# Kernel optimization log

Hardware: AMD Instinct MI355X
Metric: run time of the kernel (lower is better)

## Reference

```python
import jax, jax.numpy as jnp
import numpy as np

B, C, H, W = 8, 256, 64, 64
GROUPS = 8
EPS = 1e-5


def setup_inputs() -> dict:
    key = jax.random.key(0)
    ks = jax.random.split(key, 10)
    s = 1.0 / np.sqrt(C)
    return {
        "x": jax.random.normal(ks[0], (B, C, H, W), dtype=jnp.float32),
        "gn_gamma": jnp.ones((C,), jnp.float32),
        "gn_beta": jnp.zeros((C,), jnp.float32),
        "wq": jax.random.uniform(ks[1], (C, C), jnp.float32, -s, s),
        "bq": jax.random.uniform(ks[2], (C,), jnp.float32, -s, s),
        "wk": jax.random.uniform(ks[3], (C, C), jnp.float32, -s, s),
        "bk": jax.random.uniform(ks[4], (C,), jnp.float32, -s, s),
        "wv": jax.random.uniform(ks[5], (C, C), jnp.float32, -s, s),
        "bv": jax.random.uniform(ks[6], (C,), jnp.float32, -s, s),
        "wp": jax.random.uniform(ks[7], (C, C), jnp.float32, -s, s),
        "bp": jax.random.uniform(ks[8], (C,), jnp.float32, -s, s),
    }


def _group_norm(x, gamma, beta):
    b, c, h, w = x.shape
    xg = x.reshape(b, GROUPS, c // GROUPS, h, w)
    mu = jnp.mean(xg, axis=(2, 3, 4), keepdims=True)
    var = jnp.mean(jnp.square(xg - mu), axis=(2, 3, 4), keepdims=True)
    xn = ((xg - mu) * jax.lax.rsqrt(var + EPS)).reshape(b, c, h, w)
    return xn * gamma[None, :, None, None] + beta[None, :, None, None]


def reference(x, gn_gamma, gn_beta, wq, bq, wk, bk, wv, bv, wp, bp):
    b, c, h, w = x.shape
    xn = _group_norm(x, gn_gamma, gn_beta)
    xf = xn.reshape(b, c, h * w)  # [b, c, n]
    # 1x1 Conv1d == per-position channel matmul
    q = jnp.einsum('oc,bcn->bon', wq, xf) + bq[None, :, None]
    k = jnp.einsum('oc,bcn->bon', wk, xf) + bk[None, :, None]
    v = jnp.einsum('oc,bcn->bon', wv, xf) + bv[None, :, None]
    scale = 1.0 / jnp.sqrt(jnp.asarray(c, xf.dtype))
    # attn[b,i,j] = softmax_j(q[:,i]^T k[:,j] / sqrt(c))
    attn = jax.nn.softmax(jnp.einsum('bci,bcj->bij', q, k) * scale, axis=-1)
    # out[b,c,i] = sum_j v[b,c,j] * attn[b,i,j]
    out = jnp.einsum('bcj,bij->bci', v, attn)
    out = jnp.einsum('oc,bcn->bon', wp, out) + bp[None, :, None]
    return x + out.reshape(b, c, h, w)
```

## Files before the change

### kernel.cpp

```cpp
#include <hip/hip_runtime.h>


typedef __bf16 bf16x8 __attribute__((ext_vector_type(8)));
typedef __bf16 bf16x4 __attribute__((ext_vector_type(4)));
typedef float floatx4 __attribute__((ext_vector_type(4)));
typedef float floatx16 __attribute__((ext_vector_type(16)));

constexpr int Bb = 8, Cc_ = 256, HW = 4096;
constexpr int BNT = Bb * HW;

__device__ __forceinline__ void load_lds16(const void* g, void* l) {
  __builtin_amdgcn_global_load_lds((const __attribute__((address_space(1))) void*)g,
                                   (__attribute__((address_space(3))) void*)l, 16, 0, 0);
}

#define MEMFENCE asm volatile("" ::: "memory")
__device__ __forceinline__ void bar_sync() {
  MEMFENCE;
  __builtin_amdgcn_s_barrier();
  MEMFENCE;
}

__global__ __launch_bounds__(256) void gn_part(const float* __restrict__ x,
                                               float* __restrict__ part) {
  int sub = blockIdx.x & 7;
  int bg = blockIdx.x >> 3;
  const float4* p = (const float4*)(x + (size_t)bg * 131072 + (size_t)sub * 16384);
  int tid = threadIdx.x;
  float s = 0.f, ss = 0.f;
#pragma unroll
  for (int i = 0; i < 16; ++i) {
    float4 v = p[i * 256 + tid];
    s += v.x + v.y + v.z + v.w;
    ss += v.x * v.x + v.y * v.y + v.z * v.z + v.w * v.w;
  }
  for (int off = 32; off; off >>= 1) { s += __shfl_down(s, off); ss += __shfl_down(ss, off); }
  __shared__ float red[8];
  int wv = tid >> 6, ln = tid & 63;
  if (ln == 0) { red[wv] = s; red[4 + wv] = ss; }
  __syncthreads();
  if (tid == 0) {
    part[blockIdx.x * 2] = red[0] + red[1] + red[2] + red[3];
    part[blockIdx.x * 2 + 1] = red[4] + red[5] + red[6] + red[7];
  }
}

__global__ __launch_bounds__(256) void gn_norm_t(const float* __restrict__ x,
                                                 const float* __restrict__ part,
                                                 const float* __restrict__ gamma,
                                                 const float* __restrict__ beta,
                                                 __bf16* __restrict__ Xt) {
  __shared__ float tile[64][65];
  __shared__ float sst[4];
  int b = blockIdx.z, c0 = blockIdx.y * 64, n0 = blockIdx.x * 64;
  int tid = threadIdx.x;
  if (tid < 2) {
    int g = b * 8 + (c0 >> 5) + tid;
    float s = 0.f, ss = 0.f;
#pragma unroll
    for (int k = 0; k < 8; ++k) { s += part[(g * 8 + k) * 2]; ss += part[(g * 8 + k) * 2 + 1]; }
    float mean = s / 131072.f;
    float var = ss / 131072.f - mean * mean;
    sst[tid * 2] = mean;
    sst[tid * 2 + 1] = rsqrtf(var + 1e-5f);
  }
  int cl = tid >> 4, nl = (tid & 15) * 4;
  const float* xb = x + ((size_t)b * Cc_ + c0) * HW + n0;
#pragma unroll
  for (int i = 0; i < 4; ++i) {
    int c = cl + i * 16;
    float4 v = *(const float4*)&xb[(size_t)c * HW + nl];
    tile[c][nl] = v.x; tile[c][nl + 1] = v.y; tile[c][nl + 2] = v.z; tile[c][nl + 3] = v.w;
  }
  __syncthreads();
#pragma unroll
  for (int i = 0; i < 16; ++i) {
    int idx = i * 256 + tid;
    int n = idx >> 6, c = idx & 63;
    int gc = c0 + c;
    float mean = sst[(c >> 5) * 2], rstd = sst[(c >> 5) * 2 + 1];
    float v = (tile[c][n] - mean) * rstd * gamma[gc] + beta[gc];
    Xt[((size_t)b * HW + n0 + n) * Cc_ + gc] = (__bf16)v;
  }
}

__global__ __launch_bounds__(256) void pack_w(const float* __restrict__ wq, const float* __restrict__ wk,
                                              const float* __restrict__ wv, const float* __restrict__ wp,
                                              const float* __restrict__ bq, const float* __restrict__ bk,
                                              const float* __restrict__ bv, const float* __restrict__ bp,
                                              __bf16* __restrict__ Wqk, __bf16* __restrict__ Wv,
                                              __bf16* __restrict__ Wp, float* __restrict__ Bqk,
                                              float* __restrict__ Bv, float* __restrict__ Bp) {
  int i = blockIdx.x * 256 + threadIdx.x;
  if (i < 65536) {
    Wqk[i] = (__bf16)wq[i];
    Wqk[65536 + i] = (__bf16)wk[i];
    Wv[i] = (__bf16)wv[i];
    Wp[i] = (__bf16)wp[i];
  }
  if (i < 256) { Bqk[i] = bq[i]; Bqk[256 + i] = bk[i]; Bv[i] = bv[i]; Bp[i] = bp[i]; }
}

template <int BM, int BN, int WM, int WN, int EPI>
__global__ __launch_bounds__(256) void gemm_bt(
    const __bf16* __restrict__ A, int lda,
    const __bf16* __restrict__ B, int ldb,
    __bf16* __restrict__ C, int ldc,
    int K, float scale,
    const float* __restrict__ bias,
    const float* __restrict__ resid,
    float* __restrict__ outF) {
  constexpr int TM = WM / 16, TN = WN / 16;
  __shared__ __bf16 As[BM * 32];
  __shared__ __bf16 Bs[BN * 32];

  const int tid = threadIdx.x;
  const int wave = tid >> 6, lane = tid & 63;
  const int wr = wave >> 1, wc = wave & 1;
  const int quad = lane >> 4, l16 = lane & 15;
  const int m0 = blockIdx.y * BM, n0 = blockIdx.x * BN;
  const int srow = lane >> 2;
  const int scol = (lane & 3) * 8;

  floatx4 acc[TM][TN] = {};

  const int kTiles = K / 32;
  for (int kt = 0; kt < kTiles; ++kt) {
    const int k0 = kt * 32;
    __syncthreads();
#pragma unroll
    for (int i = 0; i < BM / 64; ++i) {
      int row = i * 64 + wave * 16 + srow;
      load_lds16(A + (size_t)(m0 + row) * lda + k0 + scol, &As[(i * 64 + wave * 16) * 32]);
    }
#pragma unroll
    for (int i = 0; i < BN / 64; ++i) {
      int row = i * 64 + wave * 16 + srow;
      load_lds16(B + (size_t)(n0 + row) * ldb + k0 + scol, &Bs[(i * 64 + wave * 16) * 32]);
    }
    __syncthreads();

    bf16x8 af[TM], bfr[TN];
#pragma unroll
    for (int i = 0; i < TM; ++i)
      af[i] = *(const bf16x8*)&As[(wr * WM + i * 16 + l16) * 32 + quad * 8];
#pragma unroll
    for (int j = 0; j < TN; ++j)
      bfr[j] = *(const bf16x8*)&Bs[(wc * WN + j * 16 + l16) * 32 + quad * 8];
#pragma unroll
    for (int i = 0; i < TM; ++i)
#pragma unroll
      for (int j = 0; j < TN; ++j)
        acc[i][j] = __builtin_amdgcn_mfma_f32_16x16x32_bf16(af[i], bfr[j], acc[i][j], 0, 0, 0);
  }

#pragma unroll
  for (int i = 0; i < TM; ++i) {
#pragma unroll
    for (int j = 0; j < TN; ++j) {
      int gc = n0 + wc * WN + j * 16 + l16;
#pragma unroll
      for (int r = 0; r < 4; ++r) {
        int gr = m0 + wr * WM + i * 16 + quad * 4 + r;
        float v = acc[i][j][r] * scale;
        if constexpr (EPI == 1) v += bias[gc];
        if constexpr (EPI == 2) v += bias[gr];
        if constexpr (EPI == 3) {
          int bb = gc >> 12, nn = gc & 4095;
          size_t oidx = (size_t)bb * (Cc_ * HW) + (size_t)gr * HW + nn;
          outF[oidx] = v + bias[gr] + resid[oidx];
        } else {
          C[(size_t)gr * ldc + gc] = (__bf16)v;
        }
      }
    }
  }
}

__global__ __launch_bounds__(256, 2) void flash_attn(const __bf16* __restrict__ QK,
                                                     const __bf16* __restrict__ V,
                                                     __bf16* __restrict__ O) {
  __shared__ __align__(16) __bf16 smem[40960];
  __bf16* Ks = smem;
  __bf16* Vt = smem + 16384;
  __bf16* Pb = smem + 32768;

  const int tid = threadIdx.x;
  const int w = tid >> 6, lane = tid & 63;
  const int l31 = lane & 31, hh = lane >> 5;
  const int b = blockIdx.x & 7;
  const int m0 = (blockIdx.x >> 3) * 64;

  if (w < 2) {
    const int h = w;
    const int ks_slot = lane & 31, ks_rin = lane >> 5;

    bf16x8 qf[2][16];
#pragma unroll
    for (int qt = 0; qt < 2; ++qt) {
      const size_t qrow = (size_t)(b * HW + m0 + qt * 32 + l31);
#pragma unroll
      for (int kc = 0; kc < 16; ++kc) {
        qf[qt][kc] = *(const bf16x8*)&QK[qrow * 512 + kc * 16 + hh * 8];
#pragma unroll
        for (int e = 0; e < 8; ++e) qf[qt][kc][e] = (__bf16)((float)qf[qt][kc][e] * 0.0625f);
      }
    }
#pragma unroll
    for (int i = 0; i < 16; ++i) {
      int rl = h * 32 + i * 2 + ks_rin;
      load_lds16(QK + (size_t)(b * HW + rl) * 512 + 256 + ((ks_slot ^ (rl & 31)) << 3),
                 &Ks[(h * 32 + i * 2) * 256]);
    }
    bar_sync();

    float lr0 = 0.f, lr1 = 0.f;
    const int jl = h * 32 + l31;
    const __bf16* krow = &Ks[jl * 256];
    const int jx = l31;

    for (int t = 0; t < 64; ++t) {
      asm volatile("s_waitcnt vmcnt(0)" ::: "memory");
      floatx16 s0 = {}, s1 = {};
      __builtin_amdgcn_s_setprio(1);
#pragma unroll
      for (int kc = 0; kc < 16; ++kc) {
        bf16x8 kfv = *(const bf16x8*)&krow[((kc * 2 + hh) ^ jx) << 3];
        s0 = __builtin_amdgcn_mfma_f32_32x32x16_bf16(kfv, qf[0][kc], s0, 0, 0, 0);
        s1 = __builtin_amdgcn_mfma_f32_32x32x16_bf16(kfv, qf[1][kc], s1, 0, 0, 0);
      }
      __builtin_amdgcn_s_setprio(0);
      asm volatile("s_waitcnt lgkmcnt(0)" ::: "memory");
      if (t < 63) {
#pragma unroll
        for (int i = 0; i < 16; ++i) {
          int rl = h * 32 + i * 2 + ks_rin;
          load_lds16(QK + (size_t)(b * HW + (t + 1) * 64 + rl) * 512 + 256 +
                         ((ks_slot ^ (rl & 31)) << 3),
                     &Ks[(h * 32 + i * 2) * 256]);
        }
      }
      float ls0 = 0.f, ls1 = 0.f;
#pragma unroll
      for (int i = 0; i < 16; ++i) {
        float p0 = __expf(s0[i]); s0[i] = p0; ls0 += p0;
        float p1 = __expf(s1[i]); s1[i] = p1; ls1 += p1;
      }
      lr0 += ls0; lr1 += ls1;
      __bf16* Pt = Pb + ((t & 1) << 12);
#pragma unroll
      for (int g = 0; g < 4; ++g) {
        bf16x4 pk0, pk1;
#pragma unroll
        for (int k = 0; k < 4; ++k) { pk0[k] = (__bf16)s0[g * 4 + k]; pk1[k] = (__bf16)s1[g * 4 + k]; }
        *(bf16x4*)&Pt[(l31) * 64 + ((((4 * h + g) ^ (l31 & 7)) << 3) + 4 * hh)] = pk0;
        *(bf16x4*)&Pt[(32 + l31) * 64 + ((((4 * h + g) ^ (l31 & 7)) << 3) + 4 * hh)] = pk1;
      }
      asm volatile("s_waitcnt lgkmcnt(0)" ::: "memory");
      bar_sync();
    }

    float* Lb = (float*)(smem + 32768);
    float l20 = lr0 + __shfl_xor(lr0, 32);
    float l21 = lr1 + __shfl_xor(lr1, 32);
    if (hh == 0) { Lb[h * 64 + l31] = l20; Lb[h * 64 + 32 + l31] = l21; }
    asm volatile("s_waitcnt lgkmcnt(0)" ::: "memory");
    bar_sync();
    if (w == 0) Lb[128 + lane] = 1.f / (Lb[lane] + Lb[64 + lane]);
    asm volatile("s_waitcnt lgkmcnt(0)" ::: "memory");
    bar_sync();
    bar_sync();
  } else {
    const int ch = w - 2;
    const int vt_slot = lane & 7, vt_rin = lane >> 3;

#pragma unroll
    for (int i = 0; i < 16; ++i) {
      int cl = ch * 128 + i * 8 + vt_rin;
      load_lds16(V + (size_t)cl * BNT + (b * HW + ((vt_slot ^ (cl & 7)) << 3)),
                 &Vt[(ch * 128 + i * 8) * 64]);
    }
    bar_sync();

    floatx16 oacc[2][4] = {};

    for (int t = 0; t < 64; ++t) {
      asm volatile("s_waitcnt vmcnt(0)" ::: "memory");
      if (t > 0) {
        const __bf16* Pp = Pb + (((t - 1) & 1) << 12);
        __builtin_amdgcn_s_setprio(1);
#pragma unroll
        for (int ks = 0; ks < 4; ++ks) {
          bf16x8 pf0 = *(const bf16x8*)&Pp[(l31) * 64 + (((ks * 2 + hh) ^ (l31 & 7)) << 3)];
          bf16x8 pf1 = *(const bf16x8*)&Pp[(32 + l31) * 64 + (((ks * 2 + hh) ^ (l31 & 7)) << 3)];
#pragma unroll
          for (int nt = 0; nt < 4; ++nt) {
            int cl = ch * 128 + nt * 32 + l31;
            bf16x8 vf = *(const bf16x8*)&Vt[cl * 64 + (((ks * 2 + hh) ^ (cl & 7)) << 3)];
            oacc[0][nt] = __builtin_amdgcn_mfma_f32_32x32x16_bf16(pf0, vf, oacc[0][nt], 0, 0, 0);
            oacc[1][nt] = __builtin_amdgcn_mfma_f32_32x32x16_bf16(pf1, vf, oacc[1][nt], 0, 0, 0);
          }
        }
        __builtin_amdgcn_s_setprio(0);
        asm volatile("s_waitcnt lgkmcnt(0)" ::: "memory");
#pragma unroll
        for (int i = 0; i < 16; ++i) {
          int cl = ch * 128 + i * 8 + vt_rin;
          load_lds16(V + (size_t)cl * BNT + (b * HW + t * 64 + ((vt_slot ^ (cl & 7)) << 3)),
                     &Vt[(ch * 128 + i * 8) * 64]);
        }
      }
      bar_sync();
    }

    asm volatile("s_waitcnt vmcnt(0)" ::: "memory");
    {
      const __bf16* Pp = Pb + 4096;
      __builtin_amdgcn_s_setprio(1);
#pragma unroll
      for (int ks = 0; ks < 4; ++ks) {
        bf16x8 pf0 = *(const bf16x8*)&Pp[(l31) * 64 + (((ks * 2 + hh) ^ (l31 & 7)) << 3)];
        bf16x8 pf1 = *(const bf16x8*)&Pp[(32 + l31) * 64 + (((ks * 2 + hh) ^ (l31 & 7)) << 3)];
#pragma unroll
        for (int nt = 0; nt < 4; ++nt) {
          int cl = ch * 128 + nt * 32 + l31;
          bf16x8 vf = *(const bf16x8*)&Vt[cl * 64 + (((ks * 2 + hh) ^ (cl & 7)) << 3)];
          oacc[0][nt] = __builtin_amdgcn_mfma_f32_32x32x16_bf16(pf0, vf, oacc[0][nt], 0, 0, 0);
          oacc[1][nt] = __builtin_amdgcn_mfma_f32_32x32x16_bf16(pf1, vf, oacc[1][nt], 0, 0, 0);
        }
      }
      __builtin_amdgcn_s_setprio(0);
    }
    asm volatile("s_waitcnt lgkmcnt(0)" ::: "memory");
    bar_sync();
    bar_sync();

    const float* Linv = (const float*)(smem + 32768) + 128;
    __bf16* Os = smem;
#pragma unroll
    for (int qt = 0; qt < 2; ++qt) {
#pragma unroll
      for (int g = 0; g < 4; ++g) {
        floatx4 lv = *(const floatx4*)&Linv[qt * 32 + g * 8 + 4 * hh];
#pragma unroll
        for (int k = 0; k < 4; ++k) {
          int qloc = qt * 32 + g * 8 + 4 * hh + k;
#pragma unroll
          for (int nt = 0; nt < 4; ++nt) {
            int c = ch * 128 + nt * 32 + l31;
            Os[qloc * 256 + c] = (__bf16)(oacc[qt][nt][g * 4 + k] * lv[k]);
          }
        }
      }
    }
    asm volatile("s_waitcnt lgkmcnt(0)" ::: "memory");
    bar_sync();
  }

  const float4* src = (const float4*)smem;
  float4* dst = (float4*)(O + (size_t)(b * HW + m0) * 256);
#pragma unroll
  for (int i = 0; i < 8; ++i) dst[i * 256 + tid] = src[i * 256 + tid];
}

extern "C" void kernel_launch(void* const* d_in, const int* in_sizes, int n_in,
                              void* d_out, int out_size, void* d_ws, size_t ws_size,
                              hipStream_t stream) {
  const float* x = (const float*)d_in[0];
  const float* gamma = (const float*)d_in[1];
  const float* beta = (const float*)d_in[2];
  const float* wq = (const float*)d_in[3];
  const float* bq = (const float*)d_in[4];
  const float* wk = (const float*)d_in[5];
  const float* bk = (const float*)d_in[6];
  const float* wv = (const float*)d_in[7];
  const float* bv = (const float*)d_in[8];
  const float* wp = (const float*)d_in[9];
  const float* bp = (const float*)d_in[10];
  float* out = (float*)d_out;

  char* ws = (char*)d_ws;
  size_t off = 0;
  auto alloc = [&](size_t n) { size_t o = off; off = (off + n + 255) & ~(size_t)255; return o; };
  __bf16* XT = (__bf16*)(ws + alloc((size_t)BNT * Cc_ * 2));
  __bf16* QK = (__bf16*)(ws + alloc((size_t)BNT * 512 * 2));
  __bf16* V  = (__bf16*)(ws + alloc((size_t)Cc_ * BNT * 2));
  __bf16* O  = (__bf16*)(ws + alloc((size_t)BNT * Cc_ * 2));
  __bf16* WQK = (__bf16*)(ws + alloc(512 * 256 * 2));
  __bf16* WV  = (__bf16*)(ws + alloc(256 * 256 * 2));
  __bf16* WP  = (__bf16*)(ws + alloc(256 * 256 * 2));
  float* BQK = (float*)(ws + alloc(512 * 4));
  float* BV  = (float*)(ws + alloc(256 * 4));
  float* BP  = (float*)(ws + alloc(256 * 4));
  float* PART = (float*)(ws + alloc(512 * 2 * 4));

  pack_w<<<dim3(256), dim3(256), 0, stream>>>(wq, wk, wv, wp, bq, bk, bv, bp,
                                              WQK, WV, WP, BQK, BV, BP);
  gn_part<<<dim3(512), dim3(256), 0, stream>>>(x, PART);
  gn_norm_t<<<dim3(64, 4, 8), dim3(256), 0, stream>>>(x, PART, gamma, beta, XT);

  gemm_bt<128, 128, 64, 64, 1><<<dim3(512 / 128, BNT / 128), dim3(256), 0, stream>>>(
      XT, 256, WQK, 256, QK, 512, 256, 1.0f, BQK, nullptr, nullptr);
  gemm_bt<128, 128, 64, 64, 2><<<dim3(BNT / 128, 256 / 128), dim3(256), 0, stream>>>(
      WV, 256, XT, 256, V, BNT, 256, 1.0f, BV, nullptr, nullptr);

  flash_attn<<<dim3(512), dim3(256), 0, stream>>>(QK, V, O);

  gemm_bt<128, 128, 64, 64, 3><<<dim3(BNT / 128, 256 / 128), dim3(256), 0, stream>>>(
      WP, 256, O, 256, nullptr, 0, 256, 1.0f, BP, x, out);
}
```

Before: 316.4 us.

## Double query tile per block and double-buffer K tiles in flash attention

The flash attention block now covers 128 query rows with 512 threads (4 QK warps, 4 PV warps), so each K and V tile loaded into LDS serves twice as many queries. K tiles are double-buffered, with the next tile's load issued before the current tile's MFMAs instead of after. The PV warps now each cover 64 channels across 4 query subtiles. LDS use rises to 128KB per block and the grid halves to 256 blocks, which may reduce occupancy and concurrency.

```diff
diff --git a/kernel.cpp b/kernel.cpp
--- a/kernel.cpp
+++ b/kernel.cpp
@@ -177,28 +177,28 @@
   }
 }
 
-__global__ __launch_bounds__(256, 2) void flash_attn(const __bf16* __restrict__ QK,
+__global__ __launch_bounds__(512, 2) void flash_attn(const __bf16* __restrict__ QK,
                                                      const __bf16* __restrict__ V,
                                                      __bf16* __restrict__ O) {
-  __shared__ __align__(16) __bf16 smem[40960];
+  __shared__ __align__(16) __bf16 smem[65536];
   __bf16* Ks = smem;
-  __bf16* Vt = smem + 16384;
-  __bf16* Pb = smem + 32768;
+  __bf16* Vt = smem + 32768;
+  __bf16* Pb = smem + 49152;
 
   const int tid = threadIdx.x;
   const int w = tid >> 6, lane = tid & 63;
   const int l31 = lane & 31, hh = lane >> 5;
   const int b = blockIdx.x & 7;
-  const int m0 = (blockIdx.x >> 3) * 64;
-
-  if (w < 2) {
-    const int h = w;
+  const int m0 = (blockIdx.x >> 3) * 128;
+
+  if (w < 4) {
+    const int h = w & 1, qp = w >> 1;
     const int ks_slot = lane & 31, ks_rin = lane >> 5;
 
     bf16x8 qf[2][16];
 #pragma unroll
     for (int qt = 0; qt < 2; ++qt) {
-      const size_t qrow = (size_t)(b * HW + m0 + qt * 32 + l31);
+      const size_t qrow = (size_t)(b * HW + m0 + qp * 64 + qt * 32 + l31);
 #pragma unroll
       for (int kc = 0; kc < 16; ++kc) {
         qf[qt][kc] = *(const bf16x8*)&QK[qrow * 512 + kc * 16 + hh * 8];
@@ -207,39 +207,38 @@
       }
     }
 #pragma unroll
-    for (int i = 0; i < 16; ++i) {
-      int rl = h * 32 + i * 2 + ks_rin;
+    for (int i = 0; i < 8; ++i) {
+      int rl = w * 16 + i * 2 + ks_rin;
       load_lds16(QK + (size_t)(b * HW + rl) * 512 + 256 + ((ks_slot ^ (rl & 31)) << 3),
-                 &Ks[(h * 32 + i * 2) * 256]);
-    }
+                 &Ks[(w * 16 + i * 2) * 256]);
+    }
+    asm volatile("s_waitcnt vmcnt(0)" ::: "memory");
     bar_sync();
 
     float lr0 = 0.f, lr1 = 0.f;
     const int jl = h * 32 + l31;
-    const __bf16* krow = &Ks[jl * 256];
-    const int jx = l31;
 
     for (int t = 0; t < 64; ++t) {
-      asm volatile("s_waitcnt vmcnt(0)" ::: "memory");
+      if (t < 63) {
+        __bf16* Kn = Ks + (((t + 1) & 1) << 14);
+#pragma unroll
+        for (int i = 0; i < 8; ++i) {
+          int rl = w * 16 + i * 2 + ks_rin;
+          load_lds16(QK + (size_t)(b * HW + (t + 1) * 64 + rl) * 512 + 256 +
+                         ((ks_slot ^ (rl & 31)) << 3),
+                     &Kn[(w * 16 + i * 2) * 256]);
+        }
+      }
+      const __bf16* krow = &Ks[((t & 1) << 14) + jl * 256];
       floatx16 s0 = {}, s1 = {};
       __builtin_amdgcn_s_setprio(1);
 #pragma unroll
       for (int kc = 0; kc < 16; ++kc) {
-        bf16x8 kfv = *(const bf16x8*)&krow[((kc * 2 + hh) ^ jx) << 3];
+        bf16x8 kfv = *(const bf16x8*)&krow[((kc * 2 + hh) ^ l31) << 3];
         s0 = __builtin_amdgcn_mfma_f32_32x32x16_bf16(kfv, qf[0][kc], s0, 0, 0, 0);
         s1 = __builtin_amdgcn_mfma_f32_32x32x16_bf16(kfv, qf[1][kc], s1, 0, 0, 0);
       }
       __builtin_amdgcn_s_setprio(0);
-      asm volatile("s_waitcnt lgkmcnt(0)" ::: "memory");
-      if (t < 63) {
-#pragma unroll
-        for (int i = 0; i < 16; ++i) {
-          int rl = h * 32 + i * 2 + ks_rin;
-          load_lds16(QK + (size_t)(b * HW + (t + 1) * 64 + rl) * 512 + 256 +
-                         ((ks_slot ^ (rl & 31)) << 3),
-                     &Ks[(h * 32 + i * 2) * 256]);
-        }
-      }
       float ls0 = 0.f, ls1 = 0.f;
 #pragma unroll
       for (int i = 0; i < 16; ++i) {
@@ -247,67 +246,79 @@
         float p1 = __expf(s1[i]); s1[i] = p1; ls1 += p1;
       }
       lr0 += ls0; lr1 += ls1;
-      __bf16* Pt = Pb + ((t & 1) << 12);
+      __bf16* Pt = Pb + ((t & 1) << 13);
 #pragma unroll
       for (int g = 0; g < 4; ++g) {
         bf16x4 pk0, pk1;
 #pragma unroll
         for (int k = 0; k < 4; ++k) { pk0[k] = (__bf16)s0[g * 4 + k]; pk1[k] = (__bf16)s1[g * 4 + k]; }
-        *(bf16x4*)&Pt[(l31) * 64 + ((((4 * h + g) ^ (l31 & 7)) << 3) + 4 * hh)] = pk0;
-        *(bf16x4*)&Pt[(32 + l31) * 64 + ((((4 * h + g) ^ (l31 & 7)) << 3) + 4 * hh)] = pk1;
-      }
-      asm volatile("s_waitcnt lgkmcnt(0)" ::: "memory");
+        *(bf16x4*)&Pt[(qp * 64 + l31) * 64 + ((((4 * h + g) ^ (l31 & 7)) << 3) + 4 * hh)] = pk0;
+        *(bf16x4*)&Pt[(qp * 64 + 32 + l31) * 64 + ((((4 * h + g) ^ (l31 & 7)) << 3) + 4 * hh)] = pk1;
+      }
+      asm volatile("s_waitcnt vmcnt(0) lgkmcnt(0)" ::: "memory");
       bar_sync();
     }
 
-    float* Lb = (float*)(smem + 32768);
+    float* Lb = (float*)Pb;
     float l20 = lr0 + __shfl_xor(lr0, 32);
     float l21 = lr1 + __shfl_xor(lr1, 32);
-    if (hh == 0) { Lb[h * 64 + l31] = l20; Lb[h * 64 + 32 + l31] = l21; }
+    if (hh == 0) {
+      Lb[h * 128 + qp * 64 + l31] = l20;
+      Lb[h * 128 + qp * 64 + 32 + l31] = l21;
+    }
     asm volatile("s_waitcnt lgkmcnt(0)" ::: "memory");
     bar_sync();
-    if (w == 0) Lb[128 + lane] = 1.f / (Lb[lane] + Lb[64 + lane]);
+    if (w == 0) {
+      float* Linv = (float*)Pb + 256;
+      Linv[lane] = 1.f / (Lb[lane] + Lb[128 + lane]);
+      Linv[64 + lane] = 1.f / (Lb[64 + lane] + Lb[192 + lane]);
+    }
     asm volatile("s_waitcnt lgkmcnt(0)" ::: "memory");
     bar_sync();
     bar_sync();
   } else {
-    const int ch = w - 2;
+    const int ch = w - 4;
     const int vt_slot = lane & 7, vt_rin = lane >> 3;
 
 #pragma unroll
-    for (int i = 0; i < 16; ++i) {
-      int cl = ch * 128 + i * 8 + vt_rin;
+    for (int i = 0; i < 8; ++i) {
+      int cl = ch * 64 + i * 8 + vt_rin;
       load_lds16(V + (size_t)cl * BNT + (b * HW + ((vt_slot ^ (cl & 7)) << 3)),
-                 &Vt[(ch * 128 + i * 8) * 64]);
-    }
-    bar_sync();
-
-    floatx16 oacc[2][4] = {};
+                 &Vt[(ch * 64 + i * 8) * 64]);
+    }
+    bar_sync();
+
+    floatx16 oacc[4][2] = {};
 
     for (int t = 0; t < 64; ++t) {
       asm volatile("s_waitcnt vmcnt(0)" ::: "memory");
       if (t > 0) {
-        const __bf16* Pp = Pb + (((t - 1) & 1) << 12);
+        const __bf16* Pp = Pb + (((t - 1) & 1) << 13);
         __builtin_amdgcn_s_setprio(1);
 #pragma unroll
         for (int ks = 0; ks < 4; ++ks) {
-          bf16x8 pf0 = *(const bf16x8*)&Pp[(l31) * 64 + (((ks * 2 + hh) ^ (l31 & 7)) << 3)];
-          bf16x8 pf1 = *(const bf16x8*)&Pp[(32 + l31) * 64 + (((ks * 2 + hh) ^ (l31 & 7)) << 3)];
-#pragma unroll
-          for (int nt = 0; nt < 4; ++nt) {
-            int cl = ch * 128 + nt * 32 + l31;
-            bf16x8 vf = *(const bf16x8*)&Vt[cl * 64 + (((ks * 2 + hh) ^ (cl & 7)) << 3)];
-            oacc[0][nt] = __builtin_amdgcn_mfma_f32_32x32x16_bf16(pf0, vf, oacc[0][nt], 0, 0, 0);
-            oacc[1][nt] = __builtin_amdgcn_mfma_f32_32x32x16_bf16(pf1, vf, oacc[1][nt], 0, 0, 0);
+          bf16x8 pf[4], vf[2];
+#pragma unroll
+          for (int qt = 0; qt < 4; ++qt)
+            pf[qt] = *(const bf16x8*)&Pp[(qt * 32 + l31) * 64 + (((ks * 2 + hh) ^ (l31 & 7)) << 3)];
+#pragma unroll
+          for (int nt = 0; nt < 2; ++nt) {
+            int cl = ch * 64 + nt * 32 + l31;
+            vf[nt] = *(const bf16x8*)&Vt[cl * 64 + (((ks * 2 + hh) ^ (cl & 7)) << 3)];
           }
+#pragma unroll
+          for (int qt = 0; qt < 4; ++qt)
+#pragma unroll
+            for (int nt = 0; nt < 2; ++nt)
+              oacc[qt][nt] = __builtin_amdgcn_mfma_f32_32x32x16_bf16(pf[qt], vf[nt], oacc[qt][nt], 0, 0, 0);
         }
         __builtin_amdgcn_s_setprio(0);
         asm volatile("s_waitcnt lgkmcnt(0)" ::: "memory");
 #pragma unroll
-        for (int i = 0; i < 16; ++i) {
-          int cl = ch * 128 + i * 8 + vt_rin;
+        for (int i = 0; i < 8; ++i) {
+          int cl = ch * 64 + i * 8 + vt_rin;
           load_lds16(V + (size_t)cl * BNT + (b * HW + t * 64 + ((vt_slot ^ (cl & 7)) << 3)),
-                     &Vt[(ch * 128 + i * 8) * 64]);
+                     &Vt[(ch * 64 + i * 8) * 64]);
         }
       }
       bar_sync();
@@ -315,19 +326,24 @@
 
     asm volatile("s_waitcnt vmcnt(0)" ::: "memory");
     {
-      const __bf16* Pp = Pb + 4096;
+      const __bf16* Pp = Pb + 8192;
       __builtin_amdgcn_s_setprio(1);
 #pragma unroll
       for (int ks = 0; ks < 4; ++ks) {
-        bf16x8 pf0 = *(const bf16x8*)&Pp[(l31) * 64 + (((ks * 2 + hh) ^ (l31 & 7)) << 3)];
-        bf16x8 pf1 = *(const bf16x8*)&Pp[(32 + l31) * 64 + (((ks * 2 + hh) ^ (l31 & 7)) << 3)];
-#pragma unroll
-        for (int nt = 0; nt < 4; ++nt) {
-          int cl = ch * 128 + nt * 32 + l31;
-          bf16x8 vf = *(const bf16x8*)&Vt[cl * 64 + (((ks * 2 + hh) ^ (cl & 7)) << 3)];
-          oacc[0][nt] = __builtin_amdgcn_mfma_f32_32x32x16_bf16(pf0, vf, oacc[0][nt], 0, 0, 0);
-          oacc[1][nt] = __builtin_amdgcn_mfma_f32_32x32x16_bf16(pf1, vf, oacc[1][nt], 0, 0, 0);
-        }
+        bf16x8 pf[4], vf[2];
+#pragma unroll
+        for (int qt = 0; qt < 4; ++qt)
+          pf[qt] = *(const bf16x8*)&Pp[(qt * 32 + l31) * 64 + (((ks * 2 + hh) ^ (l31 & 7)) << 3)];
+#pragma unroll
+        for (int nt = 0; nt < 2; ++nt) {
+          int cl = ch * 64 + nt * 32 + l31;
+          vf[nt] = *(const bf16x8*)&Vt[cl * 64 + (((ks * 2 + hh) ^ (cl & 7)) << 3)];
+        }
+#pragma unroll
+        for (int qt = 0; qt < 4; ++qt)
+#pragma unroll
+          for (int nt = 0; nt < 2; ++nt)
+            oacc[qt][nt] = __builtin_amdgcn_mfma_f32_32x32x16_bf16(pf[qt], vf[nt], oacc[qt][nt], 0, 0, 0);
       }
       __builtin_amdgcn_s_setprio(0);
     }
@@ -335,10 +351,10 @@
     bar_sync();
     bar_sync();
 
-    const float* Linv = (const float*)(smem + 32768) + 128;
+    const float* Linv = (const float*)Pb + 256;
     __bf16* Os = smem;
 #pragma unroll
-    for (int qt = 0; qt < 2; ++qt) {
+    for (int qt = 0; qt < 4; ++qt) {
 #pragma unroll
       for (int g = 0; g < 4; ++g) {
         floatx4 lv = *(const floatx4*)&Linv[qt * 32 + g * 8 + 4 * hh];
@@ -346,8 +362,8 @@
         for (int k = 0; k < 4; ++k) {
           int qloc = qt * 32 + g * 8 + 4 * hh + k;
 #pragma unroll
-          for (int nt = 0; nt < 4; ++nt) {
-            int c = ch * 128 + nt * 32 + l31;
+          for (int nt = 0; nt < 2; ++nt) {
+            int c = ch * 64 + nt * 32 + l31;
             Os[qloc * 256 + c] = (__bf16)(oacc[qt][nt][g * 4 + k] * lv[k]);
           }
         }
@@ -360,7 +376,7 @@
   const float4* src = (const float4*)smem;
   float4* dst = (float4*)(O + (size_t)(b * HW + m0) * 256);
 #pragma unroll
-  for (int i = 0; i < 8; ++i) dst[i * 256 + tid] = src[i * 256 + tid];
+  for (int i = 0; i < 8; ++i) dst[i * 512 + tid] = src[i * 512 + tid];
 }
 
 extern "C" void kernel_launch(void* const* d_in, const int* in_sizes, int n_in,
@@ -404,7 +420,7 @@
   gemm_bt<128, 128, 64, 64, 2><<<dim3(BNT / 128, 256 / 128), dim3(256), 0, stream>>>(
       WV, 256, XT, 256, V, BNT, 256, 1.0f, BV, nullptr, nullptr);
 
-  flash_attn<<<dim3(512), dim3(256), 0, stream>>>(QK, V, O);
+  flash_attn<<<dim3(256), dim3(512), 0, stream>>>(QK, V, O);
 
   gemm_bt<128, 128, 64, 64, 3><<<dim3(BNT / 128, 256 / 128), dim3(256), 0, stream>>>(
       WP, 256, O, 256, nullptr, 0, 256, 1.0f, BP, x, out);
```

After: 291.4 us. 1.09x faster.

## Stage K/V prefetch through registers in attention and fuse weight packing into GN stats

Applied to the files above, without the earlier changes.

The attention kernel's K and V tiles are now loaded into registers one or two iterations ahead and stored to swizzled LDS after compute. This replaces async global-to-LDS loads that required a vmcnt(0) wait at the top of each iteration, so more global latency can be hidden behind the MFMA work. The weight packing kernel is merged into the group-norm partial-sum kernel as extra blocks, saving one launch. In exchange, each thread holds 16 extra vector registers, which may reduce occupancy or cause spills.

```diff
diff --git a/kernel.cpp b/kernel.cpp
--- a/kernel.cpp
+++ b/kernel.cpp
@@ -21,27 +21,44 @@
   MEMFENCE;
 }
 
-__global__ __launch_bounds__(256) void gn_part(const float* __restrict__ x,
-                                               float* __restrict__ part) {
-  int sub = blockIdx.x & 7;
-  int bg = blockIdx.x >> 3;
-  const float4* p = (const float4*)(x + (size_t)bg * 131072 + (size_t)sub * 16384);
+__global__ __launch_bounds__(256) void gn_part_pack(
+    const float* __restrict__ x, float* __restrict__ part,
+    const float* __restrict__ wq, const float* __restrict__ wk,
+    const float* __restrict__ wv, const float* __restrict__ wp,
+    const float* __restrict__ bq, const float* __restrict__ bk,
+    const float* __restrict__ bv, const float* __restrict__ bp,
+    __bf16* __restrict__ Wqk, __bf16* __restrict__ Wv, __bf16* __restrict__ Wp,
+    float* __restrict__ Bqk, float* __restrict__ Bv, float* __restrict__ Bp) {
+  __shared__ float red[8];
   int tid = threadIdx.x;
-  float s = 0.f, ss = 0.f;
-#pragma unroll
-  for (int i = 0; i < 16; ++i) {
-    float4 v = p[i * 256 + tid];
-    s += v.x + v.y + v.z + v.w;
-    ss += v.x * v.x + v.y * v.y + v.z * v.z + v.w * v.w;
-  }
-  for (int off = 32; off; off >>= 1) { s += __shfl_down(s, off); ss += __shfl_down(ss, off); }
-  __shared__ float red[8];
-  int wv = tid >> 6, ln = tid & 63;
-  if (ln == 0) { red[wv] = s; red[4 + wv] = ss; }
-  __syncthreads();
-  if (tid == 0) {
-    part[blockIdx.x * 2] = red[0] + red[1] + red[2] + red[3];
-    part[blockIdx.x * 2 + 1] = red[4] + red[5] + red[6] + red[7];
+  if (blockIdx.x < 512) {
+    int sub = blockIdx.x & 7;
+    int bg = blockIdx.x >> 3;
+    const float4* p = (const float4*)(x + (size_t)bg * 131072 + (size_t)sub * 16384);
+    float s = 0.f, ss = 0.f;
+#pragma unroll
+    for (int i = 0; i < 16; ++i) {
+      float4 v = p[i * 256 + tid];
+      s += v.x + v.y + v.z + v.w;
+      ss += v.x * v.x + v.y * v.y + v.z * v.z + v.w * v.w;
+    }
+    for (int off = 32; off; off >>= 1) { s += __shfl_down(s, off); ss += __shfl_down(ss, off); }
+    int wv_ = tid >> 6, ln = tid & 63;
+    if (ln == 0) { red[wv_] = s; red[4 + wv_] = ss; }
+    __syncthreads();
+    if (tid == 0) {
+      part[blockIdx.x * 2] = red[0] + red[1] + red[2] + red[3];
+      part[blockIdx.x * 2 + 1] = red[4] + red[5] + red[6] + red[7];
+    }
+  } else {
+    int i = (blockIdx.x - 512) * 256 + tid;
+    if (i < 65536) {
+      Wqk[i] = (__bf16)wq[i];
+      Wqk[65536 + i] = (__bf16)wk[i];
+      Wv[i] = (__bf16)wv[i];
+      Wp[i] = (__bf16)wp[i];
+    }
+    if (i < 256) { Bqk[i] = bq[i]; Bqk[256 + i] = bk[i]; Bv[i] = bv[i]; Bp[i] = bp[i]; }
   }
 }
 
@@ -84,23 +101,6 @@
   }
 }
 
-__global__ __launch_bounds__(256) void pack_w(const float* __restrict__ wq, const float* __restrict__ wk,
-                                              const float* __restrict__ wv, const float* __restrict__ wp,
-                                              const float* __restrict__ bq, const float* __restrict__ bk,
-                                              const float* __restrict__ bv, const float* __restrict__ bp,
-                                              __bf16* __restrict__ Wqk, __bf16* __restrict__ Wv,
-                                              __bf16* __restrict__ Wp, float* __restrict__ Bqk,
-                                              float* __restrict__ Bv, float* __restrict__ Bp) {
-  int i = blockIdx.x * 256 + threadIdx.x;
-  if (i < 65536) {
-    Wqk[i] = (__bf16)wq[i];
-    Wqk[65536 + i] = (__bf16)wk[i];
-    Wv[i] = (__bf16)wv[i];
-    Wp[i] = (__bf16)wp[i];
-  }
-  if (i < 256) { Bqk[i] = bq[i]; Bqk[256 + i] = bk[i]; Bv[i] = bv[i]; Bp[i] = bp[i]; }
-}
-
 template <int BM, int BN, int WM, int WN, int EPI>
 __global__ __launch_bounds__(256) void gemm_bt(
     const __bf16* __restrict__ A, int lda,
@@ -206,26 +206,35 @@
         for (int e = 0; e < 8; ++e) qf[qt][kc][e] = (__bf16)((float)qf[qt][kc][e] * 0.0625f);
       }
     }
+    bf16x8 kreg[16];
 #pragma unroll
     for (int i = 0; i < 16; ++i) {
       int rl = h * 32 + i * 2 + ks_rin;
-      load_lds16(QK + (size_t)(b * HW + rl) * 512 + 256 + ((ks_slot ^ (rl & 31)) << 3),
-                 &Ks[(h * 32 + i * 2) * 256]);
-    }
+      kreg[i] = *(const bf16x8*)&QK[(size_t)(b * HW + rl) * 512 + 256 + ks_slot * 8];
+    }
+#pragma unroll
+    for (int i = 0; i < 16; ++i) {
+      int rl = h * 32 + i * 2 + ks_rin;
+      *(bf16x8*)&Ks[rl * 256 + ((ks_slot ^ (rl & 31)) << 3)] = kreg[i];
+    }
+#pragma unroll
+    for (int i = 0; i < 16; ++i) {
+      int rl = h * 32 + i * 2 + ks_rin;
+      kreg[i] = *(const bf16x8*)&QK[(size_t)(b * HW + 64 + rl) * 512 + 256 + ks_slot * 8];
+    }
+    asm volatile("s_waitcnt lgkmcnt(0)" ::: "memory");
     bar_sync();
 
     float lr0 = 0.f, lr1 = 0.f;
     const int jl = h * 32 + l31;
     const __bf16* krow = &Ks[jl * 256];
-    const int jx = l31;
 
     for (int t = 0; t < 64; ++t) {
-      asm volatile("s_waitcnt vmcnt(0)" ::: "memory");
       floatx16 s0 = {}, s1 = {};
       __builtin_amdgcn_s_setprio(1);
 #pragma unroll
       for (int kc = 0; kc < 16; ++kc) {
-        bf16x8 kfv = *(const bf16x8*)&krow[((kc * 2 + hh) ^ jx) << 3];
+        bf16x8 kfv = *(const bf16x8*)&krow[((kc * 2 + hh) ^ l31) << 3];
         s0 = __builtin_amdgcn_mfma_f32_32x32x16_bf16(kfv, qf[0][kc], s0, 0, 0, 0);
         s1 = __builtin_amdgcn_mfma_f32_32x32x16_bf16(kfv, qf[1][kc], s1, 0, 0, 0);
       }
@@ -235,9 +244,14 @@
 #pragma unroll
         for (int i = 0; i < 16; ++i) {
           int rl = h * 32 + i * 2 + ks_rin;
-          load_lds16(QK + (size_t)(b * HW + (t + 1) * 64 + rl) * 512 + 256 +
-                         ((ks_slot ^ (rl & 31)) << 3),
-                     &Ks[(h * 32 + i * 2) * 256]);
+          *(bf16x8*)&Ks[rl * 256 + ((ks_slot ^ (rl & 31)) << 3)] = kreg[i];
+        }
+      }
+      if (t < 62) {
+#pragma unroll
+        for (int i = 0; i < 16; ++i) {
+          int rl = h * 32 + i * 2 + ks_rin;
+          kreg[i] = *(const bf16x8*)&QK[(size_t)(b * HW + (t + 2) * 64 + rl) * 512 + 256 + ks_slot * 8];
         }
       }
       float ls0 = 0.f, ls1 = 0.f;
@@ -274,18 +288,17 @@
     const int ch = w - 2;
     const int vt_slot = lane & 7, vt_rin = lane >> 3;
 
+    bf16x8 vreg[16];
 #pragma unroll
     for (int i = 0; i < 16; ++i) {
       int cl = ch * 128 + i * 8 + vt_rin;
-      load_lds16(V + (size_t)cl * BNT + (b * HW + ((vt_slot ^ (cl & 7)) << 3)),
-                 &Vt[(ch * 128 + i * 8) * 64]);
+      vreg[i] = *(const bf16x8*)&V[(size_t)cl * BNT + b * HW + vt_slot * 8];
     }
     bar_sync();
 
     floatx16 oacc[2][4] = {};
 
     for (int t = 0; t < 64; ++t) {
-      asm volatile("s_waitcnt vmcnt(0)" ::: "memory");
       if (t > 0) {
         const __bf16* Pp = Pb + (((t - 1) & 1) << 12);
         __builtin_amdgcn_s_setprio(1);
@@ -303,17 +316,23 @@
         }
         __builtin_amdgcn_s_setprio(0);
         asm volatile("s_waitcnt lgkmcnt(0)" ::: "memory");
+      }
+#pragma unroll
+      for (int i = 0; i < 16; ++i) {
+        int cl = ch * 128 + i * 8 + vt_rin;
+        *(bf16x8*)&Vt[cl * 64 + ((vt_slot ^ (cl & 7)) << 3)] = vreg[i];
+      }
+      if (t < 63) {
 #pragma unroll
         for (int i = 0; i < 16; ++i) {
           int cl = ch * 128 + i * 8 + vt_rin;
-          load_lds16(V + (size_t)cl * BNT + (b * HW + t * 64 + ((vt_slot ^ (cl & 7)) << 3)),
-                     &Vt[(ch * 128 + i * 8) * 64]);
-        }
-      }
+          vreg[i] = *(const bf16x8*)&V[(size_t)cl * BNT + b * HW + (t + 1) * 64 + vt_slot * 8];
+        }
+      }
+      asm volatile("s_waitcnt lgkmcnt(0)" ::: "memory");
       bar_sync();
     }
 
-    asm volatile("s_waitcnt vmcnt(0)" ::: "memory");
     {
       const __bf16* Pp = Pb + 4096;
       __builtin_amdgcn_s_setprio(1);
@@ -394,9 +413,9 @@
   float* BP  = (float*)(ws + alloc(256 * 4));
   float* PART = (float*)(ws + alloc(512 * 2 * 4));
 
-  pack_w<<<dim3(256), dim3(256), 0, stream>>>(wq, wk, wv, wp, bq, bk, bv, bp,
-                                              WQK, WV, WP, BQK, BV, BP);
-  gn_part<<<dim3(512), dim3(256), 0, stream>>>(x, PART);
+  gn_part_pack<<<dim3(768), dim3(256), 0, stream>>>(x, PART, wq, wk, wv, wp,
+                                                    bq, bk, bv, bp,
+                                                    WQK, WV, WP, BQK, BV, BP);
   gn_norm_t<<<dim3(64, 4, 8), dim3(256), 0, stream>>>(x, PART, gamma, beta, XT);
 
   gemm_bt<128, 128, 64, 64, 1><<<dim3(512 / 128, BNT / 128), dim3(256), 0, stream>>>(
```

New measurement: 364.9 us. 1.15x slower.
